# Kernel tuning notes

Measured on AMD Instinct MI355X. Metric: run time of the kernel, lower is better.

Reference implementation:

```python
import jax, jax.numpy as jnp
import numpy as np

N, CF, NC, H, W = 8, 32, 2, 512, 512
R0, R1 = 100, 228           # 128x128 foreground rectangle -> K = 16384 pixels
K = (R1 - R0) * (R1 - R0)
GAMMA = 0.9                 # cosine-similarity pseudo-label threshold (torch default)
BETA = 0.5                  # fisher-loss weight (torch default is 0; nonzero to exercise term)


def setup_inputs() -> dict:
    key = jax.random.key(0)
    k1, k2 = jax.random.split(key)
    tgt = np.zeros((N, H, W), np.int32)
    tgt[:, R0:R1, R0:R1] = 1
    flat = tgt[0].reshape(-1)
    fg = np.where(flat == 1)[0].astype(np.int32)          # (K,) same rect every item
    bg_cand = np.where(flat == 0)[0]
    rng = np.random.default_rng(0)
    # mirrors host-side np.random.choice(..., replace=False) of K background pixels per item
    bg = np.stack([rng.choice(bg_cand, K, replace=False) for _ in range(N)]).astype(np.int32)
    fg = np.tile(fg[None], (N, 1))
    return {
        "activ_last_layer": jax.random.normal(k1, (N, CF, H, W), jnp.float32),
        "predict": jax.random.normal(k2, (N, NC, H, W), jnp.float32),
        "target": jnp.asarray(tgt),
        "full_target": jnp.asarray(tgt),
        "fg_idx": jnp.asarray(fg),
        "bg_idx": jnp.asarray(bg),
        "t": 50, "T1": 10, "T2": 100, "lam": 1,
    }


def _per_item(act, pred, tgt, fg, bg):
    HW = H * W
    act_f = act.reshape(CF, HW)                         # (C, HW)
    logp = jax.nn.log_softmax(pred.reshape(NC, HW).T, axis=-1)  # (HW, NC)
    tgt_f = tgt.reshape(HW)
    # supervised CE over K foreground + K sampled background pixels (mean)
    sup_idx = jnp.concatenate([fg, bg])
    loss_sup = -jnp.mean(logp[sup_idx, tgt_f[sup_idx]])
    # class centroids from gathered feature vectors
    bg_feats = act_f[:, bg]                             # (C, K)
    fg_feats = act_f[:, fg]
    c0 = bg_feats.mean(axis=1)
    c1 = fg_feats.mean(axis=1)
    act_norm = jnp.linalg.norm(act_f, axis=0)           # (HW,)
    n0 = jnp.linalg.norm(c0)
    n1 = jnp.linalg.norm(c1)
    sim0 = (c0 @ act_f) / (n0 * act_norm)               # cosine_sim, (HW,)
    sim1 = (c1 @ act_f) / (n1 * act_norm)
    # torch sets pseudo=0 where sim0>gamma, then overwrites with 1 where sim1>gamma
    pseudo = jnp.where(sim1 > GAMMA, 1, jnp.where(sim0 > GAMMA, 0, 2))
    mask = (tgt_f == 0)
    mask = mask.at[bg].set(False)
    mask = mask & (pseudo != 2)
    ce_pseudo = -jnp.take_along_axis(logp, jnp.clip(pseudo, 0, NC - 1)[:, None], axis=1)[:, 0]
    m = mask.astype(logp.dtype)
    loss_self = jnp.sum(ce_pseudo * m) / jnp.sum(m)
    # fisher ratio pieces (faithful to torch expressions, including odd denominators)
    fnum = jnp.sum(c0 * c1) / (n0 * n1)
    sym0 = (c0 @ bg_feats) / jnp.linalg.norm(c0 * jnp.linalg.norm(bg_feats, axis=1))
    sym1 = (c1 @ fg_feats) / jnp.linalg.norm(c1 * jnp.linalg.norm(fg_feats, axis=1))
    fden = jnp.sum(sym0) + jnp.sum(sym1)
    return loss_sup, loss_self, fnum, fden


def reference(activ_last_layer, predict, target, full_target, fg_idx, bg_idx, t, T1, T2, lam):
    ls, lss, fn, fd = jax.vmap(_per_item)(activ_last_layer, predict, target, fg_idx, bg_idx)
    loss_sup = jnp.sum(ls)
    loss_self = jnp.sum(lss)
    loss_fisher = jnp.sum(fn) / jnp.sum(fd)
    if t < T1:
        return loss_sup
    alpha = (t - T1) * lam / (T2 - T1) if t < T2 else lam
    loss = loss_sup + alpha * loss_self + BETA * loss_fisher
    return jnp.where(jnp.isnan(loss_self) | jnp.isnan(loss_fisher), loss_sup, loss)
```

## Files before the change

kernel.cpp:

```cpp
#include <hip/hip_runtime.h>
#include <math.h>

#define HW   262144
#define NCF  32
#define NB   8
#define KK   16384
#define GAMMA 0.9f
#define BETA  0.5f

#define WS_C0SUM   0
#define WS_C1SUM   256
#define WS_R0SQ    512
#define WS_R1SQ    768
#define WS_SUP     1024
#define WS_SELFNUM 1032
#define WS_SELFDEN 1040
#define WS_FNUM    1048
#define WS_FDEN    1056
#define WS_C0      1064
#define WS_C1      1320
#define WS_N0      1576
#define WS_N1      1584
#define WS_MASK_F  8192

__global__ __launch_bounds__(256) void scatter_bg(const int* __restrict__ bg,
                                                  unsigned char* __restrict__ mask) {
    int i = blockIdx.x * 256 + threadIdx.x;
    int n = i >> 14;
    mask[(size_t)n * HW + bg[i]] = 1;
}

__global__ __launch_bounds__(256) void centroid_sums(const float* __restrict__ act,
                                                     const int* __restrict__ fg,
                                                     const int* __restrict__ bg,
                                                     float* __restrict__ ws) {
    int b = blockIdx.x;
    int c = b & 31;
    int s = (b >> 5) & 1;
    int n = b >> 6;
    const int* idx = (s ? fg : bg) + n * KK;
    const float* plane = act + (size_t)(n * NCF + c) * HW;
    float sum = 0.f, sq = 0.f;
    for (int k = threadIdx.x * 4; k < KK; k += 1024) {
        int4 id = *(const int4*)(idx + k);
        float a0 = plane[id.x], a1 = plane[id.y], a2 = plane[id.z], a3 = plane[id.w];
        sum += (a0 + a1) + (a2 + a3);
        sq  += a0*a0 + a1*a1 + a2*a2 + a3*a3;
    }
    __shared__ float red[2][4];
    for (int m = 32; m >= 1; m >>= 1) { sum += __shfl_xor(sum, m); sq += __shfl_xor(sq, m); }
    int lane = threadIdx.x & 63, wid = threadIdx.x >> 6;
    if (lane == 0) { red[0][wid] = sum; red[1][wid] = sq; }
    __syncthreads();
    if (threadIdx.x == 0) {
        sum = red[0][0] + red[0][1] + red[0][2] + red[0][3];
        sq  = red[1][0] + red[1][1] + red[1][2] + red[1][3];
        ws[(s ? WS_C1SUM : WS_C0SUM) + n * 32 + c] = sum;
        ws[(s ? WS_R1SQ  : WS_R0SQ ) + n * 32 + c] = sq;
    }
}

__global__ __launch_bounds__(64) void finalize_centroids(float* __restrict__ ws) {
    int n = blockIdx.x;
    int c = threadIdx.x & 31;
    float c0 = ws[WS_C0SUM + n * 32 + c] * (1.0f / KK);
    float c1 = ws[WS_C1SUM + n * 32 + c] * (1.0f / KK);
    float r0sq = ws[WS_R0SQ + n * 32 + c];
    float r1sq = ws[WS_R1SQ + n * 32 + c];
    float s_t0 = c0 * c0 * r0sq;
    float s_t1 = c1 * c1 * r1sq;
    float s_n0 = c0 * c0, s_n1 = c1 * c1, s_dot = c0 * c1;
    for (int m = 16; m >= 1; m >>= 1) {
        s_t0 += __shfl_xor(s_t0, m); s_t1 += __shfl_xor(s_t1, m);
        s_n0 += __shfl_xor(s_n0, m); s_n1 += __shfl_xor(s_n1, m);
        s_dot += __shfl_xor(s_dot, m);
    }
    if (threadIdx.x < 32) {
        ws[WS_C0 + n * 32 + c] = c0;
        ws[WS_C1 + n * 32 + c] = c1;
        if (c == 0) {
            float n0 = sqrtf(s_n0), n1 = sqrtf(s_n1);
            ws[WS_N0 + n] = n0;
            ws[WS_N1 + n] = n1;
            ws[WS_FNUM + n] = s_dot / (n0 * n1);
            ws[WS_FDEN + n] = (float)KK * s_n0 / sqrtf(s_t0)
                            + (float)KK * s_n1 / sqrtf(s_t1);
        }
    }
}

__global__ __launch_bounds__(256) void main_pass(const float* __restrict__ act,
                                                 const float* __restrict__ pred,
                                                 const int* __restrict__ tgt,
                                                 const unsigned char* __restrict__ mask,
                                                 float* __restrict__ ws) {
    int n = blockIdx.x >> 8;
    int base = ((blockIdx.x & 255) << 10) | (threadIdx.x << 2);
    const float* aplane = act + (size_t)n * NCF * HW + base;

    __shared__ float sc0[32], sc1[32];
    if (threadIdx.x < 32) {
        sc0[threadIdx.x] = ws[WS_C0 + n * 32 + threadIdx.x];
        sc1[threadIdx.x] = ws[WS_C1 + n * 32 + threadIdx.x];
    }
    __syncthreads();
    float n0 = ws[WS_N0 + n], n1 = ws[WS_N1 + n];

    float4 d0 = {0,0,0,0}, d1 = {0,0,0,0}, nr = {0,0,0,0};
#pragma unroll
    for (int c = 0; c < 32; ++c) {
        float4 a = *(const float4*)(aplane + (size_t)c * HW);
        float w0 = sc0[c], w1 = sc1[c];
        d0.x += w0 * a.x; d0.y += w0 * a.y; d0.z += w0 * a.z; d0.w += w0 * a.w;
        d1.x += w1 * a.x; d1.y += w1 * a.y; d1.z += w1 * a.z; d1.w += w1 * a.w;
        nr.x += a.x * a.x; nr.y += a.y * a.y; nr.z += a.z * a.z; nr.w += a.w * a.w;
    }

    float dd0[4] = {d0.x, d0.y, d0.z, d0.w};
    float dd1[4] = {d1.x, d1.y, d1.z, d1.w};
    float nn[4]  = {nr.x, nr.y, nr.z, nr.w};
    int4 tv = *(const int4*)(tgt + (size_t)n * HW + base);
    int tarr[4] = {tv.x, tv.y, tv.z, tv.w};
    uchar4 mv = *(const uchar4*)(mask + (size_t)n * HW + base);
    unsigned char marr[4] = {mv.x, mv.y, mv.z, mv.w};
    const float* pp = pred + (size_t)n * 2 * HW + base;
    float4 q0 = *(const float4*)pp;
    float4 q1 = *(const float4*)(pp + HW);
    float p0a[4] = {q0.x, q0.y, q0.z, q0.w};
    float p1a[4] = {q1.x, q1.y, q1.z, q1.w};

    float sups = 0.f, sn = 0.f, sd = 0.f;
    float g0 = GAMMA * n0, g1 = GAMMA * n1;
#pragma unroll
    for (int j = 0; j < 4; ++j) {
        float an = sqrtf(nn[j]);
        int pseudo = (dd1[j] > g1 * an) ? 1 : ((dd0[j] > g0 * an) ? 0 : 2);
        float mx = fmaxf(p0a[j], p1a[j]);
        float lse = mx + logf(expf(p0a[j] - mx) + expf(p1a[j] - mx));
        float lp0 = p0a[j] - lse, lp1 = p1a[j] - lse;
        bool isbg = marr[j] != 0;
        int tg = tarr[j];
        if (tg == 1 || isbg) sups += tg ? lp1 : lp0;
        if (tg == 0 && !isbg && pseudo != 2) { sn += (pseudo == 1) ? -lp1 : -lp0; sd += 1.0f; }
    }

    __shared__ float red[3][4];
    for (int m = 32; m >= 1; m >>= 1) {
        sups += __shfl_xor(sups, m); sn += __shfl_xor(sn, m); sd += __shfl_xor(sd, m);
    }
    int lane = threadIdx.x & 63, wid = threadIdx.x >> 6;
    if (lane == 0) { red[0][wid] = sups; red[1][wid] = sn; red[2][wid] = sd; }
    __syncthreads();
    if (threadIdx.x == 0) {
        atomicAdd(&ws[WS_SUP],         red[0][0] + red[0][1] + red[0][2] + red[0][3]);
        atomicAdd(&ws[WS_SELFNUM + n], red[1][0] + red[1][1] + red[1][2] + red[1][3]);
        atomicAdd(&ws[WS_SELFDEN + n], red[2][0] + red[2][1] + red[2][2] + red[2][3]);
    }
}

__global__ __launch_bounds__(64) void final_combine(const float* __restrict__ ws,
                                                    const int* __restrict__ t_,
                                                    const int* __restrict__ T1_,
                                                    const int* __restrict__ T2_,
                                                    const int* __restrict__ lam_,
                                                    float* __restrict__ out) {
    if (threadIdx.x != 0) return;
    float sup = -ws[WS_SUP] / (float)(2 * KK);
    float self = 0.f, fn = 0.f, fd = 0.f;
    for (int n = 0; n < NB; ++n) {
        self += ws[WS_SELFNUM + n] / ws[WS_SELFDEN + n];
        fn += ws[WS_FNUM + n];
        fd += ws[WS_FDEN + n];
    }
    float fisher = fn / fd;
    int t = *t_, T1 = *T1_, T2 = *T2_;
    float lam = (float)*lam_;
    float res;
    if (t < T1) {
        res = sup;
    } else {
        float alpha = (t < T2) ? (float)(t - T1) * lam / (float)(T2 - T1) : lam;
        float loss = sup + alpha * self + BETA * fisher;
        bool bad = (self != self) || (fisher != fisher);
        res = bad ? sup : loss;
    }
    out[0] = res;
}

extern "C" void kernel_launch(void* const* d_in, const int* in_sizes, int n_in,
                              void* d_out, int out_size, void* d_ws, size_t ws_size,
                              hipStream_t stream) {
    const float* act  = (const float*)d_in[0];
    const float* pred = (const float*)d_in[1];
    const int*   tgt  = (const int*)d_in[2];
    const int*   fg   = (const int*)d_in[4];
    const int*   bg   = (const int*)d_in[5];
    const int*   t_   = (const int*)d_in[6];
    const int*   T1_  = (const int*)d_in[7];
    const int*   T2_  = (const int*)d_in[8];
    const int*   lam_ = (const int*)d_in[9];
    float* ws = (float*)d_ws;
    unsigned char* mask = (unsigned char*)d_ws + (size_t)WS_MASK_F * 4;
    float* out = (float*)d_out;

    hipMemsetAsync(d_ws, 0, (size_t)WS_MASK_F * 4 + (size_t)NB * HW, stream);
    hipLaunchKernelGGL(scatter_bg, dim3(NB * KK / 256), dim3(256), 0, stream, bg, mask);
    hipLaunchKernelGGL(centroid_sums, dim3(NB * 2 * NCF), dim3(256), 0, stream, act, fg, bg, ws);
    hipLaunchKernelGGL(finalize_centroids, dim3(NB), dim3(64), 0, stream, ws);
    hipLaunchKernelGGL(main_pass, dim3(NB * HW / 1024), dim3(256), 0, stream, act, pred, tgt, mask, ws);
    hipLaunchKernelGGL(final_combine, dim3(1), dim3(64), 0, stream, ws, t_, T1_, T2_, lam_, out);
}
```

Before: 494.4 us.

## Replace gathered centroid sums with dense coded streaming pass over activations

Builds a per-pixel byte code from the target (1 = foreground, 2 = sampled background). Centroid sums and squared sums are then accumulated by streaming each activation plane contiguously, with per-chunk atomics, instead of doing random index gathers over fg/bg lists. The main pass reads the compact code in place of the int32 target plus the mask, and the large workspace memset shrinks. It trades scattered gathers for reading the whole activation tensor one extra time. It also assumes fg_idx equals exactly the target==1 pixels.

```diff
diff --git a/kernel.cpp b/kernel.cpp
--- a/kernel.cpp
+++ b/kernel.cpp
@@ -21,42 +21,59 @@
 #define WS_C1      1320
 #define WS_N0      1576
 #define WS_N1      1584
-#define WS_MASK_F  8192
+#define WS_CODE_F  8192
+
+__global__ __launch_bounds__(256) void build_code(const int* __restrict__ tgt,
+                                                  unsigned char* __restrict__ code) {
+    int i = blockIdx.x * 1024 + threadIdx.x * 4;
+    int4 tv = *(const int4*)(tgt + i);
+    uchar4 cd;
+    cd.x = (tv.x == 1); cd.y = (tv.y == 1); cd.z = (tv.z == 1); cd.w = (tv.w == 1);
+    *(uchar4*)(code + i) = cd;
+}
 
 __global__ __launch_bounds__(256) void scatter_bg(const int* __restrict__ bg,
-                                                  unsigned char* __restrict__ mask) {
+                                                  unsigned char* __restrict__ code) {
     int i = blockIdx.x * 256 + threadIdx.x;
     int n = i >> 14;
-    mask[(size_t)n * HW + bg[i]] = 1;
-}
-
-__global__ __launch_bounds__(256) void centroid_sums(const float* __restrict__ act,
-                                                     const int* __restrict__ fg,
-                                                     const int* __restrict__ bg,
+    code[(size_t)n * HW + bg[i]] = 2;
+}
+
+__global__ __launch_bounds__(256) void centroid_pass(const float* __restrict__ act,
+                                                     const unsigned char* __restrict__ code,
                                                      float* __restrict__ ws) {
-    int b = blockIdx.x;
-    int c = b & 31;
-    int s = (b >> 5) & 1;
-    int n = b >> 6;
-    const int* idx = (s ? fg : bg) + n * KK;
-    const float* plane = act + (size_t)(n * NCF + c) * HW;
-    float sum = 0.f, sq = 0.f;
-    for (int k = threadIdx.x * 4; k < KK; k += 1024) {
-        int4 id = *(const int4*)(idx + k);
-        float a0 = plane[id.x], a1 = plane[id.y], a2 = plane[id.z], a3 = plane[id.w];
-        sum += (a0 + a1) + (a2 + a3);
-        sq  += a0*a0 + a1*a1 + a2*a2 + a3*a3;
-    }
-    __shared__ float red[2][4];
-    for (int m = 32; m >= 1; m >>= 1) { sum += __shfl_xor(sum, m); sq += __shfl_xor(sq, m); }
+    int chunk = blockIdx.x & 15;
+    int c = (blockIdx.x >> 4) & 31;
+    int n = blockIdx.x >> 9;
+    const float* plane = act + (size_t)(n * NCF + c) * HW + chunk * 16384;
+    const unsigned char* cp = code + (size_t)n * HW + chunk * 16384;
+    float s0 = 0.f, q0 = 0.f, s1 = 0.f, q1 = 0.f;
+    for (int i = threadIdx.x * 4; i < 16384; i += 1024) {
+        float4 a = *(const float4*)(plane + i);
+        uchar4 cd = *(const uchar4*)(cp + i);
+        float b;
+        b = (cd.x == 2) ? 1.f : 0.f; s0 += b * a.x; q0 += b * a.x * a.x;
+        b = (cd.x == 1) ? 1.f : 0.f; s1 += b * a.x; q1 += b * a.x * a.x;
+        b = (cd.y == 2) ? 1.f : 0.f; s0 += b * a.y; q0 += b * a.y * a.y;
+        b = (cd.y == 1) ? 1.f : 0.f; s1 += b * a.y; q1 += b * a.y * a.y;
+        b = (cd.z == 2) ? 1.f : 0.f; s0 += b * a.z; q0 += b * a.z * a.z;
+        b = (cd.z == 1) ? 1.f : 0.f; s1 += b * a.z; q1 += b * a.z * a.z;
+        b = (cd.w == 2) ? 1.f : 0.f; s0 += b * a.w; q0 += b * a.w * a.w;
+        b = (cd.w == 1) ? 1.f : 0.f; s1 += b * a.w; q1 += b * a.w * a.w;
+    }
+    __shared__ float red[4][4];
+    for (int m = 32; m >= 1; m >>= 1) {
+        s0 += __shfl_xor(s0, m); q0 += __shfl_xor(q0, m);
+        s1 += __shfl_xor(s1, m); q1 += __shfl_xor(q1, m);
+    }
     int lane = threadIdx.x & 63, wid = threadIdx.x >> 6;
-    if (lane == 0) { red[0][wid] = sum; red[1][wid] = sq; }
+    if (lane == 0) { red[0][wid] = s0; red[1][wid] = q0; red[2][wid] = s1; red[3][wid] = q1; }
     __syncthreads();
     if (threadIdx.x == 0) {
-        sum = red[0][0] + red[0][1] + red[0][2] + red[0][3];
-        sq  = red[1][0] + red[1][1] + red[1][2] + red[1][3];
-        ws[(s ? WS_C1SUM : WS_C0SUM) + n * 32 + c] = sum;
-        ws[(s ? WS_R1SQ  : WS_R0SQ ) + n * 32 + c] = sq;
+        atomicAdd(&ws[WS_C0SUM + n * 32 + c], red[0][0] + red[0][1] + red[0][2] + red[0][3]);
+        atomicAdd(&ws[WS_R0SQ  + n * 32 + c], red[1][0] + red[1][1] + red[1][2] + red[1][3]);
+        atomicAdd(&ws[WS_C1SUM + n * 32 + c], red[2][0] + red[2][1] + red[2][2] + red[2][3]);
+        atomicAdd(&ws[WS_R1SQ  + n * 32 + c], red[3][0] + red[3][1] + red[3][2] + red[3][3]);
     }
 }
 
@@ -91,8 +108,7 @@
 
 __global__ __launch_bounds__(256) void main_pass(const float* __restrict__ act,
                                                  const float* __restrict__ pred,
-                                                 const int* __restrict__ tgt,
-                                                 const unsigned char* __restrict__ mask,
+                                                 const unsigned char* __restrict__ code,
                                                  float* __restrict__ ws) {
     int n = blockIdx.x >> 8;
     int base = ((blockIdx.x & 255) << 10) | (threadIdx.x << 2);
@@ -119,9 +135,7 @@
     float dd0[4] = {d0.x, d0.y, d0.z, d0.w};
     float dd1[4] = {d1.x, d1.y, d1.z, d1.w};
     float nn[4]  = {nr.x, nr.y, nr.z, nr.w};
-    int4 tv = *(const int4*)(tgt + (size_t)n * HW + base);
-    int tarr[4] = {tv.x, tv.y, tv.z, tv.w};
-    uchar4 mv = *(const uchar4*)(mask + (size_t)n * HW + base);
+    uchar4 mv = *(const uchar4*)(code + (size_t)n * HW + base);
     unsigned char marr[4] = {mv.x, mv.y, mv.z, mv.w};
     const float* pp = pred + (size_t)n * 2 * HW + base;
     float4 q0 = *(const float4*)pp;
@@ -138,10 +152,9 @@
         float mx = fmaxf(p0a[j], p1a[j]);
         float lse = mx + logf(expf(p0a[j] - mx) + expf(p1a[j] - mx));
         float lp0 = p0a[j] - lse, lp1 = p1a[j] - lse;
-        bool isbg = marr[j] != 0;
-        int tg = tarr[j];
-        if (tg == 1 || isbg) sups += tg ? lp1 : lp0;
-        if (tg == 0 && !isbg && pseudo != 2) { sn += (pseudo == 1) ? -lp1 : -lp0; sd += 1.0f; }
+        unsigned char cd = marr[j];
+        if (cd != 0) sups += (cd == 1) ? lp1 : lp0;
+        if (cd == 0 && pseudo != 2) { sn += (pseudo == 1) ? -lp1 : -lp0; sd += 1.0f; }
     }
 
     __shared__ float red[3][4];
@@ -193,20 +206,21 @@
     const float* act  = (const float*)d_in[0];
     const float* pred = (const float*)d_in[1];
     const int*   tgt  = (const int*)d_in[2];
-    const int*   fg   = (const int*)d_in[4];
+    const int*   fg   = (const int*)d_in[4];  (void)fg;
     const int*   bg   = (const int*)d_in[5];
     const int*   t_   = (const int*)d_in[6];
     const int*   T1_  = (const int*)d_in[7];
     const int*   T2_  = (const int*)d_in[8];
     const int*   lam_ = (const int*)d_in[9];
     float* ws = (float*)d_ws;
-    unsigned char* mask = (unsigned char*)d_ws + (size_t)WS_MASK_F * 4;
+    unsigned char* code = (unsigned char*)d_ws + (size_t)WS_CODE_F * 4;
     float* out = (float*)d_out;
 
-    hipMemsetAsync(d_ws, 0, (size_t)WS_MASK_F * 4 + (size_t)NB * HW, stream);
-    hipLaunchKernelGGL(scatter_bg, dim3(NB * KK / 256), dim3(256), 0, stream, bg, mask);
-    hipLaunchKernelGGL(centroid_sums, dim3(NB * 2 * NCF), dim3(256), 0, stream, act, fg, bg, ws);
+    hipMemsetAsync(d_ws, 0, 8192, stream);
+    hipLaunchKernelGGL(build_code, dim3(NB * HW / 1024), dim3(256), 0, stream, tgt, code);
+    hipLaunchKernelGGL(scatter_bg, dim3(NB * KK / 256), dim3(256), 0, stream, bg, code);
+    hipLaunchKernelGGL(centroid_pass, dim3(NB * NCF * 16), dim3(256), 0, stream, act, code, ws);
     hipLaunchKernelGGL(finalize_centroids, dim3(NB), dim3(64), 0, stream, ws);
-    hipLaunchKernelGGL(main_pass, dim3(NB * HW / 1024), dim3(256), 0, stream, act, pred, tgt, mask, ws);
+    hipLaunchKernelGGL(main_pass, dim3(NB * HW / 1024), dim3(256), 0, stream, act, pred, code, ws);
     hipLaunchKernelGGL(final_combine, dim3(1), dim3(64), 0, stream, ws, t_, T1_, T2_, lam_, out);
 }
```

New measurement: 469.7 us (median of 2 runs). 1.05x faster.
